# Performance work log

Hardware: AMD Instinct MI355X
Metric: run time of the kernel (lower is better)

## Reference

```python
import jax, jax.numpy as jnp
import numpy as np

N_HEADS = 16
HEAD_DIM = 64
HIDDEN = 1024


def setup_inputs() -> dict:
    key = jax.random.key(0)
    kx, kq, kk, kv, ko = jax.random.split(key, 5)
    B, S = 1, 4096
    # xavier_uniform for Linear(hidden, n_heads*head_dim): limit = sqrt(6/(fan_in+fan_out))
    lim = float(np.sqrt(6.0 / (HIDDEN + N_HEADS * HEAD_DIM)))
    x = jax.random.normal(kx, (B, S, HIDDEN), dtype=jnp.float32)
    wq = jax.random.uniform(kq, (N_HEADS * HEAD_DIM, HIDDEN), jnp.float32, -lim, lim)
    wk = jax.random.uniform(kk, (N_HEADS * HEAD_DIM, HIDDEN), jnp.float32, -lim, lim)
    wv = jax.random.uniform(kv, (N_HEADS * HEAD_DIM, HIDDEN), jnp.float32, -lim, lim)
    wo = jax.random.uniform(ko, (HIDDEN, N_HEADS * HEAD_DIM), jnp.float32, -lim, lim)
    return {"x": x, "wq": wq, "wk": wk, "wv": wv, "wo": wo}


def reference(x, wq, wk, wv, wo):
    B, S, _ = x.shape
    scale = HEAD_DIM ** -0.5
    # project and split heads: [B, H, S, D]
    def proj(w):
        return jnp.einsum('bsh,eh->bse', x, w).reshape(B, S, N_HEADS, HEAD_DIM).transpose(0, 2, 1, 3)
    q, k, v = proj(wq), proj(wk), proj(wv)
    scores = jnp.einsum('bhqd,bhkd->bhqk', q, k) * scale  # [B,H,S,S]
    causal = jnp.tril(jnp.ones((S, S), dtype=bool))
    scores = jnp.where(causal, scores, -jnp.inf)
    probs = jax.nn.softmax(scores, axis=-1)
    out = jnp.einsum('bhqk,bhkd->bhqd', probs, v)  # [B,H,S,D]
    out = out.transpose(0, 2, 1, 3).reshape(B, S, N_HEADS * HEAD_DIM)
    return jnp.einsum('bse,he->bsh', out, wo)
```

## Files before the change

kernel.cpp:

```cpp
#include <hip/hip_runtime.h>
#include <hip/hip_bf16.h>
#include <stdint.h>

typedef unsigned short u16;
typedef float f32x4 __attribute__((ext_vector_type(4)));
typedef __bf16 bf16x8 __attribute__((ext_vector_type(8)));
typedef u16 u16x8 __attribute__((ext_vector_type(8)));

#define GL2LDS16(g, l)                                                          \
  __builtin_amdgcn_global_load_lds(                                             \
      (const __attribute__((address_space(1))) unsigned int*)(g),               \
      (__attribute__((address_space(3))) unsigned int*)(l), 16, 0, 0)

#if __has_builtin(__builtin_amdgcn_exp2f)
#define EXP2(x) __builtin_amdgcn_exp2f(x)
#else
#define EXP2(x) exp2f(x)
#endif

#define SOFTMAX_SC 0.18033688f

__device__ __forceinline__ u16 f2bf(float f) {
  uint32_t u = __builtin_bit_cast(uint32_t, f);
  return (u16)((u + 0x7FFFu + ((u >> 16) & 1u)) >> 16);
}

__device__ __forceinline__ float bf2f(u16 b) {
  return __builtin_bit_cast(float, (uint32_t)b << 16);
}

__device__ __forceinline__ uint32_t cvt_pk_bf16(float lo, float hi) {
  uint32_t r;
  asm("v_cvt_pk_bf16_f32 %0, %1, %2" : "=v"(r) : "v"(lo), "v"(hi));
  return r;
}

__device__ __forceinline__ void cast8(const float* __restrict__ s,
                                      u16* __restrict__ d) {
  const float4* p = (const float4*)s;
  float4 a = p[0], b = p[1];
  uint4 o;
  o.x = cvt_pk_bf16(a.x, a.y);
  o.y = cvt_pk_bf16(a.z, a.w);
  o.z = cvt_pk_bf16(b.x, b.y);
  o.w = cvt_pk_bf16(b.z, b.w);
  *(uint4*)d = o;
}

__global__ __launch_bounds__(256) void castall_kernel(
    const float* __restrict__ x, const float* __restrict__ wq,
    const float* __restrict__ wk, const float* __restrict__ wv,
    const float* __restrict__ wo, u16* __restrict__ xb,
    u16* __restrict__ wqkv) {
  int b = blockIdx.x;
  if (b < 2048) {
    int i = (b * 256 + threadIdx.x) * 8;
    cast8(x + i, xb + i);
  } else {
    b -= 2048;
    int w = b >> 9;
    int i = ((b & 511) * 256 + threadIdx.x) * 8;
    const float* s = (w == 0) ? wq : (w == 1) ? wk : (w == 2) ? wv : wo;
    cast8(s + i, wqkv + ((size_t)w << 20) + i);
  }
}

template <int MB>
__device__ __forceinline__ void mfma16(f32x4 (&acc)[8][4], const bf16x8 (&af)[4],
                                       const bf16x8 (&bfr)[4]) {
  asm volatile("s_waitcnt lgkmcnt(0)" ::: "memory");
  __builtin_amdgcn_sched_barrier(0);
  __builtin_amdgcn_s_setprio(1);
#pragma unroll
  for (int j = 0; j < 4; ++j)
#pragma unroll
    for (int n = 0; n < 4; ++n)
      acc[MB + j][n] = __builtin_amdgcn_mfma_f32_16x16x32_bf16(
          af[j], bfr[n], acc[MB + j][n], 0, 0, 0);
  __builtin_amdgcn_s_setprio(0);
}

__global__ __launch_bounds__(512, 2) void gemm8k(const u16* __restrict__ A,
                                                 const u16* __restrict__ B,
                                                 u16* __restrict__ qb,
                                                 u16* __restrict__ kb,
                                                 u16* __restrict__ vt) {
  const int K = 1024;
  __shared__ u16 As[4][128 * 64];
  __shared__ u16 Bs[4][128 * 64];
  const int tid = threadIdx.x;
  const int lane = tid & 63;
  const int l15 = lane & 15, lhi = lane >> 4;
  const int wave = tid >> 6;
  const int wm = wave >> 2, wn = wave & 3;
  int bid = blockIdx.y * gridDim.x + blockIdx.x;
  const int cpx = (gridDim.x * gridDim.y) >> 3;
  bid = (bid & 7) * cpx + (bid >> 3);
  const int m0 = (bid / gridDim.x) * 256, n0 = (bid % gridDim.x) * 256;
  const int nt = K >> 6;

  int aoff[2][8], boff[2][4];
#pragma unroll
  for (int ks = 0; ks < 2; ++ks) {
    const int sl = ((ks * 4 + lhi) ^ (l15 & 7)) << 4;
#pragma unroll
    for (int m = 0; m < 8; ++m) aoff[ks][m] = (m * 16 + l15) * 128 + sl;
#pragma unroll
    for (int n = 0; n < 4; ++n)
      boff[ks][n] = ((wn & 1) * 64 + n * 16 + l15) * 128 + sl;
  }

  auto stA = [&](int T, int h) {
    u16* lb = As[(T & 1) * 2 + h];
#pragma unroll
    for (int i = 0; i < 2; ++i) {
      int c = tid + i * 512;
      int row = c >> 3;
      int scol = ((c & 7) ^ (row & 7)) * 8;
      GL2LDS16(A + (size_t)(m0 + h * 128 + row) * K + T * 64 + scol,
               (char*)lb + c * 16);
    }
  };
  auto stB = [&](int T, int h) {
    u16* lb = Bs[(T & 1) * 2 + h];
#pragma unroll
    for (int i = 0; i < 2; ++i) {
      int c = tid + i * 512;
      int row = c >> 3;
      int scol = ((c & 7) ^ (row & 7)) * 8;
      GL2LDS16(B + (size_t)(n0 + h * 128 + row) * K + T * 64 + scol,
               (char*)lb + c * 16);
    }
  };

  f32x4 acc[8][4] = {};

  stA(0, 0); stA(0, 1); stB(0, 0); stB(0, 1);
  asm volatile("s_waitcnt vmcnt(0)" ::: "memory");
  __builtin_amdgcn_s_barrier();

  for (int i = 0; i < nt / 2; ++i) {
    const int e = 2 * i, o = e + 1;
    const char* Ae = (const char*)As[wm];
    const char* Be = (const char*)Bs[wn >> 1];
    const char* Ao = (const char*)As[2 + wm];
    const char* Bo = (const char*)Bs[2 + (wn >> 1)];
    bf16x8 af[4], bfr[4];
    const bool pre = (e + 2) < nt;

    stA(o, 0); stA(o, 1);
    asm volatile("s_waitcnt vmcnt(4)" ::: "memory");
    __builtin_amdgcn_s_barrier();
#pragma unroll
    for (int j = 0; j < 4; ++j) af[j] = *(const bf16x8*)(Ae + aoff[0][j]);
#pragma unroll
    for (int n = 0; n < 4; ++n) bfr[n] = *(const bf16x8*)(Be + boff[0][n]);
    mfma16<0>(acc, af, bfr);
    __builtin_amdgcn_s_barrier();
#pragma unroll
    for (int j = 0; j < 4; ++j) af[j] = *(const bf16x8*)(Ae + aoff[0][4 + j]);
    stB(o, 0); stB(o, 1);
    __builtin_amdgcn_s_barrier();
    mfma16<4>(acc, af, bfr);
    __builtin_amdgcn_s_barrier();
#pragma unroll
    for (int j = 0; j < 4; ++j) af[j] = *(const bf16x8*)(Ae + aoff[1][j]);
#pragma unroll
    for (int n = 0; n < 4; ++n) bfr[n] = *(const bf16x8*)(Be + boff[1][n]);
    __builtin_amdgcn_s_barrier();
    mfma16<0>(acc, af, bfr);
    __builtin_amdgcn_s_barrier();
#pragma unroll
    for (int j = 0; j < 4; ++j) af[j] = *(const bf16x8*)(Ae + aoff[1][4 + j]);
    __builtin_amdgcn_s_barrier();
    mfma16<4>(acc, af, bfr);
    __builtin_amdgcn_s_barrier();
    if (pre) {
      stA(e + 2, 0); stA(e + 2, 1);
      asm volatile("s_waitcnt vmcnt(4)" ::: "memory");
    } else {
      asm volatile("s_waitcnt vmcnt(0)" ::: "memory");
    }
    __builtin_amdgcn_s_barrier();
#pragma unroll
    for (int j = 0; j < 4; ++j) af[j] = *(const bf16x8*)(Ao + aoff[0][j]);
#pragma unroll
    for (int n = 0; n < 4; ++n) bfr[n] = *(const bf16x8*)(Bo + boff[0][n]);
    mfma16<0>(acc, af, bfr);
    __builtin_amdgcn_s_barrier();
#pragma unroll
    for (int j = 0; j < 4; ++j) af[j] = *(const bf16x8*)(Ao + aoff[0][4 + j]);
    if (pre) { stB(e + 2, 0); stB(e + 2, 1); }
    __builtin_amdgcn_s_barrier();
    mfma16<4>(acc, af, bfr);
    __builtin_amdgcn_s_barrier();
#pragma unroll
    for (int j = 0; j < 4; ++j) af[j] = *(const bf16x8*)(Ao + aoff[1][j]);
#pragma unroll
    for (int n = 0; n < 4; ++n) bfr[n] = *(const bf16x8*)(Bo + boff[1][n]);
    __builtin_amdgcn_s_barrier();
    mfma16<0>(acc, af, bfr);
    __builtin_amdgcn_s_barrier();
#pragma unroll
    for (int j = 0; j < 4; ++j) af[j] = *(const bf16x8*)(Ao + aoff[1][4 + j]);
    __builtin_amdgcn_s_barrier();
    mfma16<4>(acc, af, bfr);
    __builtin_amdgcn_s_barrier();
  }

#pragma unroll
  for (int m = 0; m < 8; ++m) {
    int rbase = m0 + wm * 128 + m * 16 + lhi * 4;
#pragma unroll
    for (int n = 0; n < 4; ++n) {
      int col = n0 + wn * 64 + n * 16 + l15;
      if (col >= 2048) {
        uint2 pk;
        pk.x = cvt_pk_bf16(acc[m][n][0], acc[m][n][1]);
        pk.y = cvt_pk_bf16(acc[m][n][2], acc[m][n][3]);
        *(uint2*)(vt + (size_t)(col - 2048) * 4096 + rbase) = pk;
      } else {
        u16* dst = (col < 1024) ? qb : kb;
        int cc = col & 1023;
        float sc = (col < 1024) ? SOFTMAX_SC : 1.0f;
#pragma unroll
        for (int r = 0; r < 4; ++r)
          dst[(size_t)(rbase + r) * 1024 + cc] = f2bf(acc[m][n][r] * sc);
      }
    }
  }
}

__global__ __launch_bounds__(256) void gemm2p(const u16* __restrict__ A,
                                              const u16* __restrict__ B,
                                              float* __restrict__ C, int M,
                                              int N, int K) {
  __shared__ u16 As[2][128 * 64];
  __shared__ u16 Bs[2][128 * 64];
  const int tid = threadIdx.x;
  const int lane = tid & 63;
  const int l15 = lane & 15, lhi = lane >> 4;
  const int wave = tid >> 6;
  const int wr = (wave >> 1) * 64, wc = (wave & 1) * 64;
  const int m0 = blockIdx.y * 128, n0 = blockIdx.x * 128;
  const int nt = K >> 6;

  int aoff[2][4], boff[2][4];
#pragma unroll
  for (int ks = 0; ks < 2; ++ks) {
    const int sl = ((ks * 4 + lhi) ^ (l15 & 7)) << 4;
#pragma unroll
    for (int mi = 0; mi < 4; ++mi)
      aoff[ks][mi] = (wr + mi * 16 + l15) * 128 + sl;
#pragma unroll
    for (int ni = 0; ni < 4; ++ni)
      boff[ks][ni] = (wc + ni * 16 + l15) * 128 + sl;
  }

  auto stage = [&](int b, int t) {
#pragma unroll
    for (int i = 0; i < 4; ++i) {
      int c = tid + i * 256;
      int row = c >> 3;
      int scol = ((c & 7) ^ (row & 7)) * 8;
      GL2LDS16(A + (size_t)(m0 + row) * K + t * 64 + scol,
               (char*)(As[b]) + c * 16);
      GL2LDS16(B + (size_t)(n0 + row) * K + t * 64 + scol,
               (char*)(Bs[b]) + c * 16);
    }
  };

  f32x4 acc[4][4] = {};

  stage(0, 0);
  asm volatile("s_waitcnt vmcnt(0)" ::: "memory");
  __builtin_amdgcn_s_barrier();

  int cur = 0;
  for (int t = 0; t < nt; ++t) {
    if (t + 1 < nt) stage(cur ^ 1, t + 1);
    const char* Ab = (const char*)(As[cur]);
    const char* Bb = (const char*)(Bs[cur]);
#pragma unroll
    for (int ks = 0; ks < 2; ++ks) {
      bf16x8 af[4], bfr[4];
#pragma unroll
      for (int mi = 0; mi < 4; ++mi)
        af[mi] = *(const bf16x8*)(Ab + aoff[ks][mi]);
#pragma unroll
      for (int ni = 0; ni < 4; ++ni)
        bfr[ni] = *(const bf16x8*)(Bb + boff[ks][ni]);
#pragma unroll
      for (int mi = 0; mi < 4; ++mi)
#pragma unroll
        for (int ni = 0; ni < 4; ++ni)
          acc[mi][ni] = __builtin_amdgcn_mfma_f32_16x16x32_bf16(
              af[mi], bfr[ni], acc[mi][ni], 0, 0, 0);
    }
    asm volatile("s_waitcnt vmcnt(0)" ::: "memory");
    __builtin_amdgcn_s_barrier();
    cur ^= 1;
  }

#pragma unroll
  for (int mi = 0; mi < 4; ++mi) {
    int rbase = m0 + wr + mi * 16 + lhi * 4;
#pragma unroll
    for (int ni = 0; ni < 4; ++ni) {
      int col = n0 + wc + ni * 16 + l15;
#pragma unroll
      for (int r = 0; r < 4; ++r)
        C[(size_t)(rbase + r) * N + col] = acc[mi][ni][r];
    }
  }
}

__global__ __launch_bounds__(512) void attn_kernel(
    const u16* __restrict__ qb, const u16* __restrict__ kbuf,
    const u16* __restrict__ vt, u16* __restrict__ p0, u16* __restrict__ p12,
    float2* __restrict__ mlb) {
  const int h = blockIdx.y;
  const int bx = blockIdx.x;
  const int z = blockIdx.z;
  const int tid = threadIdx.x;
  const int lane = tid & 63, wave = tid >> 6;
  const int l15 = lane & 15, lhi = lane >> 4;

  u16* po = (z == 0) ? p0 : p12 + (size_t)(z - 1) * 4096 * 1024;
  float2* ml = mlb + (size_t)z * 4096 * 16;

  __shared__ u16 Ks[2][64 * 64];
  __shared__ u16 Vs[2][64 * 64];
  __shared__ u16 Ps[8][16 * 64];
  u16* Pw = Ps[wave];

  int koff[2][4];
#pragma unroll
  for (int ks = 0; ks < 2; ++ks)
#pragma unroll
    for (int nf = 0; nf < 4; ++nf) {
      int row = nf * 16 + l15;
      koff[ks][nf] = row * 128 + ((lhi * 16 + ks * 64) ^ ((row & 7) << 4));
    }
  int poff[4];
#pragma unroll
  for (int nf = 0; nf < 4; ++nf)
    poff[nf] = l15 * 128 + ((nf * 32 + lhi * 8) ^ ((l15 & 7) << 4));

  auto stage = [&](int b, int kb) {
    int c = tid;
    int row = c >> 3, slot = c & 7;
    int scol = (slot ^ (row & 7)) * 8;
    GL2LDS16(kbuf + (size_t)(kb * 64 + row) * 1024 + h * 64 + scol,
             (char*)(Ks[b]) + c * 16);
    GL2LDS16(vt + (size_t)(h * 64 + row) * 4096 + kb * 64 + scol,
             (char*)(Vs[b]) + c * 16);
  };

  int cur = 0;
  for (int rep = 0; rep < 2; ++rep) {
    const int qsb = rep ? (31 - bx) : bx;
    const int T = 2 * qsb + 2;
    const int kb0 = (z * T) / 3;
    const int kbe = ((z + 1) * T) / 3;
    const int q0 = qsb * 128 + wave * 16;

    if (kb0 >= kbe) {
      if (lhi == 0) ml[(q0 + l15) * 16 + h] = float2{-1e30f, 0.f};
      continue;
    }

    const u16* Qb = qb + (size_t)(q0 + l15) * 1024 + h * 64;
    bf16x8 qf0 = *(const bf16x8*)(const void*)(Qb + lhi * 8);
    bf16x8 qf1 = *(const bf16x8*)(const void*)(Qb + 32 + lhi * 8);

    f32x4 oa[4] = {};
    float mrow = -1e30f, lrow = 0.f;

    stage(cur, kb0);
    asm volatile("s_waitcnt vmcnt(0)" ::: "memory");
    __builtin_amdgcn_s_barrier();

    for (int kb = kb0; kb < kbe; ++kb) {
      if (kb + 1 < kbe) stage(cur ^ 1, kb + 1);

      f32x4 s[4] = {};
#pragma unroll
      for (int ks = 0; ks < 2; ++ks)
#pragma unroll
        for (int nf = 0; nf < 4; ++nf) {
          bf16x8 kf = *(const bf16x8*)((const char*)(Ks[cur]) + koff[ks][nf]);
          s[nf] = __builtin_amdgcn_mfma_f32_16x16x32_bf16(kf, ks ? qf1 : qf0,
                                                          s[nf], 0, 0, 0);
        }

      if (kb * 64 + 63 > q0) {
        const int q = q0 + l15;
#pragma unroll
        for (int nf = 0; nf < 4; ++nf)
#pragma unroll
          for (int r = 0; r < 4; ++r)
            if (kb * 64 + nf * 16 + lhi * 4 + r > q) s[nf][r] = -1e30f;
      }

      float pm0 = fmaxf(fmaxf(s[0][0], s[0][1]), fmaxf(s[0][2], s[0][3]));
      float pm1 = fmaxf(fmaxf(s[1][0], s[1][1]), fmaxf(s[1][2], s[1][3]));
      float pm2 = fmaxf(fmaxf(s[2][0], s[2][1]), fmaxf(s[2][2], s[2][3]));
      float pm3 = fmaxf(fmaxf(s[3][0], s[3][1]), fmaxf(s[3][2], s[3][3]));
      float pm = fmaxf(fmaxf(pm0, pm1), fmaxf(pm2, pm3));
      pm = fmaxf(pm, __shfl_xor(pm, 16));
      pm = fmaxf(pm, __shfl_xor(pm, 32));

      if (__any(pm - mrow > 8.0f)) {
        float mn = fmaxf(mrow, pm);
        float al = EXP2(mrow - mn);
        mrow = mn;
        lrow *= al;
        float alq[4];
#pragma unroll
        for (int r = 0; r < 4; ++r) alq[r] = __shfl(al, lhi * 4 + r, 16);
#pragma unroll
        for (int nf = 0; nf < 4; ++nf)
#pragma unroll
          for (int r = 0; r < 4; ++r) oa[nf][r] *= alq[r];
      }

#pragma unroll
      for (int nf = 0; nf < 4; ++nf)
#pragma unroll
        for (int r = 0; r < 4; ++r) s[nf][r] = EXP2(s[nf][r] - mrow);
      float rs = ((s[0][0] + s[0][1]) + (s[0][2] + s[0][3])) +
                 ((s[1][0] + s[1][1]) + (s[1][2] + s[1][3])) +
                 ((s[2][0] + s[2][1]) + (s[2][2] + s[2][3])) +
                 ((s[3][0] + s[3][1]) + (s[3][2] + s[3][3]));
      rs += __shfl_xor(rs, 16);
      rs += __shfl_xor(rs, 32);
      lrow += rs;

#pragma unroll
      for (int nf = 0; nf < 4; ++nf) {
        uint2 pk;
        pk.x = cvt_pk_bf16(s[nf][0], s[nf][1]);
        pk.y = cvt_pk_bf16(s[nf][2], s[nf][3]);
        *(uint2*)((char*)Pw + poff[nf]) = pk;
      }

      bf16x8 pf[2];
#pragma unroll
      for (int ks = 0; ks < 2; ++ks)
        pf[ks] = *(const bf16x8*)((const char*)Pw + koff[ks][0]);

#pragma unroll
      for (int ks = 0; ks < 2; ++ks)
#pragma unroll
        for (int nf = 0; nf < 4; ++nf) {
          bf16x8 vf = *(const bf16x8*)((const char*)(Vs[cur]) + koff[ks][nf]);
          oa[nf] = __builtin_amdgcn_mfma_f32_16x16x32_bf16(pf[ks], vf, oa[nf],
                                                           0, 0, 0);
        }

      asm volatile("s_waitcnt vmcnt(0)" ::: "memory");
      __builtin_amdgcn_s_barrier();
      cur ^= 1;
    }

    float linv[4];
#pragma unroll
    for (int r = 0; r < 4; ++r) {
      float lr = __shfl(lrow, lhi * 4 + r, 16);
      linv[r] = (lr > 0.f) ? 1.0f / lr : 0.f;
    }
#pragma unroll
    for (int r = 0; r < 4; ++r) {
      int rowg = q0 + lhi * 4 + r;
#pragma unroll
      for (int nf = 0; nf < 4; ++nf)
        po[(size_t)rowg * 1024 + h * 64 + nf * 16 + l15] =
            f2bf(oa[nf][r] * linv[r]);
    }
    if (lhi == 0) ml[(q0 + l15) * 16 + h] = float2{mrow, lrow};
  }
}

__global__ __launch_bounds__(256) void merge_kernel(u16* __restrict__ p0,
                                                    const u16* __restrict__ p12,
                                                    const float2* __restrict__ mlb,
                                                    int dummy) {
  int base = (blockIdx.x * 256 + threadIdx.x) * 8;
  int row = base >> 10, h = (base & 1023) >> 6;
  float2 a = mlb[row * 16 + h];
  float2 b = mlb[4096 * 16 + row * 16 + h];
  float2 c = mlb[2 * 4096 * 16 + row * 16 + h];
  float m = fmaxf(fmaxf(a.x, b.x), c.x);
  float w0 = EXP2(a.x - m) * a.y;
  float w1 = EXP2(b.x - m) * b.y;
  float w2 = EXP2(c.x - m) * c.y;
  float inv = 1.0f / (w0 + w1 + w2);
  w0 *= inv; w1 *= inv; w2 *= inv;
  u16x8 q0 = *(const u16x8*)(p0 + base);
  u16x8 q1 = *(const u16x8*)(p12 + base);
  u16x8 q2 = *(const u16x8*)(p12 + 4096 * 1024 + base);
  u16x8 o;
#pragma unroll
  for (int j = 0; j < 8; ++j)
    o[j] = f2bf(w0 * bf2f(q0[j]) + w1 * bf2f(q1[j]) + w2 * bf2f(q2[j]));
  *(u16x8*)(p0 + base) = o;
}

extern "C" void kernel_launch(void* const* d_in, const int* in_sizes, int n_in,
                              void* d_out, int out_size, void* d_ws,
                              size_t ws_size, hipStream_t stream) {
  const float* x = (const float*)d_in[0];
  const float* wq = (const float*)d_in[1];
  const float* wk = (const float*)d_in[2];
  const float* wv = (const float*)d_in[3];
  const float* wo = (const float*)d_in[4];

  u16* xb = (u16*)d_ws;
  u16* wqkv = xb + 4096 * 1024;
  u16* wob = wqkv + 3072 * 1024;
  u16* qb = wob + 1024 * 1024;
  u16* kbuf = qb + 4096 * 1024;
  u16* vt = kbuf + 4096 * 1024;
  u16* atn = vt + 4096 * 1024;
  float2* mlb = (float2*)wqkv;
  u16* p12 = (u16*)d_out;

  castall_kernel<<<4096, 256, 0, stream>>>(x, wq, wk, wv, wo, xb, wqkv);

  gemm8k<<<dim3(12, 16), 512, 0, stream>>>(xb, wqkv, qb, kbuf, vt);
  attn_kernel<<<dim3(16, 16, 3), 512, 0, stream>>>(qb, kbuf, vt, atn, p12, mlb);
  merge_kernel<<<2048, 256, 0, stream>>>(atn, p12, mlb, 0);
  gemm2p<<<dim3(8, 32), 256, 0, stream>>>(atn, wob, (float*)d_out, 4096, 1024,
                                          1024);
}
```

Measured before the change: 216.6 us.

## Pipeline attention QK/softmax across tiles, split KV in two, retune output GEMM

The attention kernel now computes the QK^T scores for tile t while running softmax and PV on tile t-1, using a three-buffer K/V ring in shared memory. It also drops the KV split from three to two halves, which simplifies the merge kernel and removes the empty-partition case. The output GEMM moves to 512 threads with 8 waves of 64x32 tiles, triple-buffered global-to-LDS loads that wait with vmcnt(4), an XCD-aware block remapping, and raised wave priority around the MFMAs. These changes aim to hide load and softmax latency behind matrix work. In exchange they use more LDS and registers and reduce the number of attention blocks.

```diff
diff --git a/kernel.cpp b/kernel.cpp
--- a/kernel.cpp
+++ b/kernel.cpp
@@ -231,36 +231,39 @@
   }
 }
 
-__global__ __launch_bounds__(256) void gemm2p(const u16* __restrict__ A,
+__global__ __launch_bounds__(512) void gemm2p(const u16* __restrict__ A,
                                               const u16* __restrict__ B,
                                               float* __restrict__ C, int M,
                                               int N, int K) {
-  __shared__ u16 As[2][128 * 64];
-  __shared__ u16 Bs[2][128 * 64];
+  __shared__ u16 As[3][128 * 64];
+  __shared__ u16 Bs[3][128 * 64];
   const int tid = threadIdx.x;
   const int lane = tid & 63;
   const int l15 = lane & 15, lhi = lane >> 4;
   const int wave = tid >> 6;
-  const int wr = (wave >> 1) * 64, wc = (wave & 1) * 64;
-  const int m0 = blockIdx.y * 128, n0 = blockIdx.x * 128;
+  const int wm = wave >> 2, wn = wave & 3;
+  int bid = blockIdx.y * gridDim.x + blockIdx.x;
+  const int cpx = (gridDim.x * gridDim.y) >> 3;
+  bid = (bid & 7) * cpx + (bid >> 3);
+  const int m0 = (bid / gridDim.x) * 128, n0 = (bid % gridDim.x) * 128;
   const int nt = K >> 6;
 
-  int aoff[2][4], boff[2][4];
+  int aoff[2][4], boff[2][2];
 #pragma unroll
   for (int ks = 0; ks < 2; ++ks) {
     const int sl = ((ks * 4 + lhi) ^ (l15 & 7)) << 4;
 #pragma unroll
     for (int mi = 0; mi < 4; ++mi)
-      aoff[ks][mi] = (wr + mi * 16 + l15) * 128 + sl;
-#pragma unroll
-    for (int ni = 0; ni < 4; ++ni)
-      boff[ks][ni] = (wc + ni * 16 + l15) * 128 + sl;
+      aoff[ks][mi] = (wm * 64 + mi * 16 + l15) * 128 + sl;
+#pragma unroll
+    for (int ni = 0; ni < 2; ++ni)
+      boff[ks][ni] = (wn * 32 + ni * 16 + l15) * 128 + sl;
   }
 
   auto stage = [&](int b, int t) {
 #pragma unroll
-    for (int i = 0; i < 4; ++i) {
-      int c = tid + i * 256;
+    for (int i = 0; i < 2; ++i) {
+      int c = tid + i * 512;
       int row = c >> 3;
       int scol = ((c & 7) ^ (row & 7)) * 8;
       GL2LDS16(A + (size_t)(m0 + row) * K + t * 64 + scol,
@@ -270,44 +273,49 @@
     }
   };
 
-  f32x4 acc[4][4] = {};
+  f32x4 acc[4][2] = {};
 
   stage(0, 0);
-  asm volatile("s_waitcnt vmcnt(0)" ::: "memory");
+  if (nt > 1) stage(1, 1);
+  if (nt > 1) asm volatile("s_waitcnt vmcnt(4)" ::: "memory");
+  else asm volatile("s_waitcnt vmcnt(0)" ::: "memory");
   __builtin_amdgcn_s_barrier();
 
-  int cur = 0;
   for (int t = 0; t < nt; ++t) {
-    if (t + 1 < nt) stage(cur ^ 1, t + 1);
-    const char* Ab = (const char*)(As[cur]);
-    const char* Bb = (const char*)(Bs[cur]);
+    if (t + 2 < nt) stage((t + 2) % 3, t + 2);
+    const char* Ab = (const char*)(As[t % 3]);
+    const char* Bb = (const char*)(Bs[t % 3]);
 #pragma unroll
     for (int ks = 0; ks < 2; ++ks) {
-      bf16x8 af[4], bfr[4];
+      bf16x8 af[4], bfr[2];
 #pragma unroll
       for (int mi = 0; mi < 4; ++mi)
         af[mi] = *(const bf16x8*)(Ab + aoff[ks][mi]);
 #pragma unroll
-      for (int ni = 0; ni < 4; ++ni)
+      for (int ni = 0; ni < 2; ++ni)
         bfr[ni] = *(const bf16x8*)(Bb + boff[ks][ni]);
+      __builtin_amdgcn_s_setprio(1);
 #pragma unroll
       for (int mi = 0; mi < 4; ++mi)
 #pragma unroll
-        for (int ni = 0; ni < 4; ++ni)
+        for (int ni = 0; ni < 2; ++ni)
           acc[mi][ni] = __builtin_amdgcn_mfma_f32_16x16x32_bf16(
               af[mi], bfr[ni], acc[mi][ni], 0, 0, 0);
-    }
-    asm volatile("s_waitcnt vmcnt(0)" ::: "memory");
-    __builtin_amdgcn_s_barrier();
-    cur ^= 1;
+      __builtin_amdgcn_s_setprio(0);
+    }
+    if (t + 1 < nt) {
+      if (t + 2 < nt) asm volatile("s_waitcnt vmcnt(4)" ::: "memory");
+      else asm volatile("s_waitcnt vmcnt(0)" ::: "memory");
+      __builtin_amdgcn_s_barrier();
+    }
   }
 
 #pragma unroll
   for (int mi = 0; mi < 4; ++mi) {
-    int rbase = m0 + wr + mi * 16 + lhi * 4;
-#pragma unroll
-    for (int ni = 0; ni < 4; ++ni) {
-      int col = n0 + wc + ni * 16 + l15;
+    int rbase = m0 + wm * 64 + mi * 16 + lhi * 4;
+#pragma unroll
+    for (int ni = 0; ni < 2; ++ni) {
+      int col = n0 + wn * 32 + ni * 16 + l15;
 #pragma unroll
       for (int r = 0; r < 4; ++r)
         C[(size_t)(rbase + r) * N + col] = acc[mi][ni][r];
@@ -317,20 +325,20 @@
 
 __global__ __launch_bounds__(512) void attn_kernel(
     const u16* __restrict__ qb, const u16* __restrict__ kbuf,
-    const u16* __restrict__ vt, u16* __restrict__ p0, u16* __restrict__ p12,
+    const u16* __restrict__ vt, u16* __restrict__ p0, u16* __restrict__ p1g,
     float2* __restrict__ mlb) {
   const int h = blockIdx.y;
   const int bx = blockIdx.x;
-  const int z = blockIdx.z;
+  const int half = blockIdx.z;
   const int tid = threadIdx.x;
   const int lane = tid & 63, wave = tid >> 6;
   const int l15 = lane & 15, lhi = lane >> 4;
 
-  u16* po = (z == 0) ? p0 : p12 + (size_t)(z - 1) * 4096 * 1024;
-  float2* ml = mlb + (size_t)z * 4096 * 16;
-
-  __shared__ u16 Ks[2][64 * 64];
-  __shared__ u16 Vs[2][64 * 64];
+  u16* po = half ? p1g : p0;
+  float2* ml = mlb + (size_t)half * 4096 * 16;
+
+  __shared__ u16 Ks[3][64 * 64];
+  __shared__ u16 Vs[3][64 * 64];
   __shared__ u16 Ps[8][16 * 64];
   u16* Pw = Ps[wave];
 
@@ -357,56 +365,45 @@
              (char*)(Vs[b]) + c * 16);
   };
 
-  int cur = 0;
   for (int rep = 0; rep < 2; ++rep) {
     const int qsb = rep ? (31 - bx) : bx;
-    const int T = 2 * qsb + 2;
-    const int kb0 = (z * T) / 3;
-    const int kbe = ((z + 1) * T) / 3;
+    const int kb0 = half * (qsb + 1);
+    const int kbe = kb0 + qsb + 1;
     const int q0 = qsb * 128 + wave * 16;
-
-    if (kb0 >= kbe) {
-      if (lhi == 0) ml[(q0 + l15) * 16 + h] = float2{-1e30f, 0.f};
-      continue;
-    }
-
     const u16* Qb = qb + (size_t)(q0 + l15) * 1024 + h * 64;
     bf16x8 qf0 = *(const bf16x8*)(const void*)(Qb + lhi * 8);
     bf16x8 qf1 = *(const bf16x8*)(const void*)(Qb + 32 + lhi * 8);
 
     f32x4 oa[4] = {};
     float mrow = -1e30f, lrow = 0.f;
-
-    stage(cur, kb0);
-    asm volatile("s_waitcnt vmcnt(0)" ::: "memory");
-    __builtin_amdgcn_s_barrier();
-
-    for (int kb = kb0; kb < kbe; ++kb) {
-      if (kb + 1 < kbe) stage(cur ^ 1, kb + 1);
-
-      f32x4 s[4] = {};
+    f32x4 sp[4];
+
+    auto qkt = [&](int buf, f32x4 (&s)[4]) {
+      __builtin_amdgcn_s_setprio(1);
 #pragma unroll
       for (int ks = 0; ks < 2; ++ks)
 #pragma unroll
         for (int nf = 0; nf < 4; ++nf) {
-          bf16x8 kf = *(const bf16x8*)((const char*)(Ks[cur]) + koff[ks][nf]);
+          bf16x8 kf = *(const bf16x8*)((const char*)(Ks[buf]) + koff[ks][nf]);
           s[nf] = __builtin_amdgcn_mfma_f32_16x16x32_bf16(kf, ks ? qf1 : qf0,
                                                           s[nf], 0, 0, 0);
         }
-
-      if (kb * 64 + 63 > q0) {
+      __builtin_amdgcn_s_setprio(0);
+    };
+
+    auto smax_pv = [&](int t, int vbuf) {
+      if (t * 64 + 63 > q0) {
         const int q = q0 + l15;
 #pragma unroll
         for (int nf = 0; nf < 4; ++nf)
 #pragma unroll
           for (int r = 0; r < 4; ++r)
-            if (kb * 64 + nf * 16 + lhi * 4 + r > q) s[nf][r] = -1e30f;
+            if (t * 64 + nf * 16 + lhi * 4 + r > q) sp[nf][r] = -1e30f;
       }
-
-      float pm0 = fmaxf(fmaxf(s[0][0], s[0][1]), fmaxf(s[0][2], s[0][3]));
-      float pm1 = fmaxf(fmaxf(s[1][0], s[1][1]), fmaxf(s[1][2], s[1][3]));
-      float pm2 = fmaxf(fmaxf(s[2][0], s[2][1]), fmaxf(s[2][2], s[2][3]));
-      float pm3 = fmaxf(fmaxf(s[3][0], s[3][1]), fmaxf(s[3][2], s[3][3]));
+      float pm0 = fmaxf(fmaxf(sp[0][0], sp[0][1]), fmaxf(sp[0][2], sp[0][3]));
+      float pm1 = fmaxf(fmaxf(sp[1][0], sp[1][1]), fmaxf(sp[1][2], sp[1][3]));
+      float pm2 = fmaxf(fmaxf(sp[2][0], sp[2][1]), fmaxf(sp[2][2], sp[2][3]));
+      float pm3 = fmaxf(fmaxf(sp[3][0], sp[3][1]), fmaxf(sp[3][2], sp[3][3]));
       float pm = fmaxf(fmaxf(pm0, pm1), fmaxf(pm2, pm3));
       pm = fmaxf(pm, __shfl_xor(pm, 16));
       pm = fmaxf(pm, __shfl_xor(pm, 32));
@@ -428,11 +425,11 @@
 #pragma unroll
       for (int nf = 0; nf < 4; ++nf)
 #pragma unroll
-        for (int r = 0; r < 4; ++r) s[nf][r] = EXP2(s[nf][r] - mrow);
-      float rs = ((s[0][0] + s[0][1]) + (s[0][2] + s[0][3])) +
-                 ((s[1][0] + s[1][1]) + (s[1][2] + s[1][3])) +
-                 ((s[2][0] + s[2][1]) + (s[2][2] + s[2][3])) +
-                 ((s[3][0] + s[3][1]) + (s[3][2] + s[3][3]));
+        for (int r = 0; r < 4; ++r) sp[nf][r] = EXP2(sp[nf][r] - mrow);
+      float rs = ((sp[0][0] + sp[0][1]) + (sp[0][2] + sp[0][3])) +
+                 ((sp[1][0] + sp[1][1]) + (sp[1][2] + sp[1][3])) +
+                 ((sp[2][0] + sp[2][1]) + (sp[2][2] + sp[2][3])) +
+                 ((sp[3][0] + sp[3][1]) + (sp[3][2] + sp[3][3]));
       rs += __shfl_xor(rs, 16);
       rs += __shfl_xor(rs, 32);
       lrow += rs;
@@ -440,29 +437,51 @@
 #pragma unroll
       for (int nf = 0; nf < 4; ++nf) {
         uint2 pk;
-        pk.x = cvt_pk_bf16(s[nf][0], s[nf][1]);
-        pk.y = cvt_pk_bf16(s[nf][2], s[nf][3]);
+        pk.x = cvt_pk_bf16(sp[nf][0], sp[nf][1]);
+        pk.y = cvt_pk_bf16(sp[nf][2], sp[nf][3]);
         *(uint2*)((char*)Pw + poff[nf]) = pk;
       }
-
       bf16x8 pf[2];
 #pragma unroll
       for (int ks = 0; ks < 2; ++ks)
         pf[ks] = *(const bf16x8*)((const char*)Pw + koff[ks][0]);
 
+      __builtin_amdgcn_s_setprio(1);
 #pragma unroll
       for (int ks = 0; ks < 2; ++ks)
 #pragma unroll
         for (int nf = 0; nf < 4; ++nf) {
-          bf16x8 vf = *(const bf16x8*)((const char*)(Vs[cur]) + koff[ks][nf]);
+          bf16x8 vf = *(const bf16x8*)((const char*)(Vs[vbuf]) + koff[ks][nf]);
           oa[nf] = __builtin_amdgcn_mfma_f32_16x16x32_bf16(pf[ks], vf, oa[nf],
                                                            0, 0, 0);
         }
-
+      __builtin_amdgcn_s_setprio(0);
+    };
+
+    stage(0, kb0);
+    asm volatile("s_waitcnt vmcnt(0)" ::: "memory");
+    __builtin_amdgcn_s_barrier();
+    if (kb0 + 1 < kbe) stage(1, kb0 + 1);
+#pragma unroll
+    for (int nf = 0; nf < 4; ++nf) sp[nf] = f32x4{0.f, 0.f, 0.f, 0.f};
+    qkt(0, sp);
+    asm volatile("s_waitcnt vmcnt(0)" ::: "memory");
+    __builtin_amdgcn_s_barrier();
+
+    for (int t = kb0 + 1; t < kbe; ++t) {
+      const int c = (t - kb0) % 3;
+      const int cp = (t - kb0 + 2) % 3;
+      const int cn = (t - kb0 + 1) % 3;
+      if (t + 1 < kbe) stage(cn, t + 1);
+      f32x4 sn[4] = {};
+      qkt(c, sn);
+      smax_pv(t - 1, cp);
       asm volatile("s_waitcnt vmcnt(0)" ::: "memory");
       __builtin_amdgcn_s_barrier();
-      cur ^= 1;
-    }
+#pragma unroll
+      for (int nf = 0; nf < 4; ++nf) sp[nf] = sn[nf];
+    }
+    smax_pv(kbe - 1, (kbe - 1 - kb0) % 3);
 
     float linv[4];
 #pragma unroll
@@ -483,27 +502,21 @@
 }
 
 __global__ __launch_bounds__(256) void merge_kernel(u16* __restrict__ p0,
-                                                    const u16* __restrict__ p12,
-                                                    const float2* __restrict__ mlb,
-                                                    int dummy) {
+                                                    const u16* __restrict__ p1,
+                                                    const float2* __restrict__ mlb) {
   int base = (blockIdx.x * 256 + threadIdx.x) * 8;
   int row = base >> 10, h = (base & 1023) >> 6;
   float2 a = mlb[row * 16 + h];
   float2 b = mlb[4096 * 16 + row * 16 + h];
-  float2 c = mlb[2 * 4096 * 16 + row * 16 + h];
-  float m = fmaxf(fmaxf(a.x, b.x), c.x);
-  float w0 = EXP2(a.x - m) * a.y;
-  float w1 = EXP2(b.x - m) * b.y;
-  float w2 = EXP2(c.x - m) * c.y;
-  float inv = 1.0f / (w0 + w1 + w2);
-  w0 *= inv; w1 *= inv; w2 *= inv;
+  float m = fmaxf(a.x, b.x);
+  float w0 = EXP2(a.x - m) * a.y, w1 = EXP2(b.x - m) * b.y;
+  float inv = 1.0f / (w0 + w1);
+  w0 *= inv; w1 *= inv;
   u16x8 q0 = *(const u16x8*)(p0 + base);
-  u16x8 q1 = *(const u16x8*)(p12 + base);
-  u16x8 q2 = *(const u16x8*)(p12 + 4096 * 1024 + base);
+  u16x8 q1 = *(const u16x8*)(p1 + base);
   u16x8 o;
 #pragma unroll
-  for (int j = 0; j < 8; ++j)
-    o[j] = f2bf(w0 * bf2f(q0[j]) + w1 * bf2f(q1[j]) + w2 * bf2f(q2[j]));
+  for (int j = 0; j < 8; ++j) o[j] = f2bf(w0 * bf2f(q0[j]) + w1 * bf2f(q1[j]));
   *(u16x8*)(p0 + base) = o;
 }
 
@@ -524,13 +537,13 @@
   u16* vt = kbuf + 4096 * 1024;
   u16* atn = vt + 4096 * 1024;
   float2* mlb = (float2*)wqkv;
-  u16* p12 = (u16*)d_out;
+  u16* p1 = (u16*)d_out;
 
   castall_kernel<<<4096, 256, 0, stream>>>(x, wq, wk, wv, wo, xb, wqkv);
 
   gemm8k<<<dim3(12, 16), 512, 0, stream>>>(xb, wqkv, qb, kbuf, vt);
-  attn_kernel<<<dim3(16, 16, 3), 512, 0, stream>>>(qb, kbuf, vt, atn, p12, mlb);
-  merge_kernel<<<2048, 256, 0, stream>>>(atn, p12, mlb, 0);
-  gemm2p<<<dim3(8, 32), 256, 0, stream>>>(atn, wob, (float*)d_out, 4096, 1024,
+  attn_kernel<<<dim3(16, 16, 2), 512, 0, stream>>>(qb, kbuf, vt, atn, p1, mlb);
+  merge_kernel<<<2048, 256, 0, stream>>>(atn, p1, mlb);
+  gemm2p<<<dim3(8, 32), 512, 0, stream>>>(atn, wob, (float*)d_out, 4096, 1024,
                                           1024);
 }
```

Result: faster. 207.9 us (-4.0%).
